# Kernel tuning notes

Measured on AMD Instinct MI355X. Metric: run time of the kernel, lower is better.

## Reference

```python
import jax, jax.numpy as jnp
import numpy as np

B, N, C_IN = 8, 2048, 2


def _pdist(x):
    # (B,N,N) pairwise euclidean distances
    d2 = jnp.sum((x[:, :, None, :] - x[:, None, :, :]) ** 2, axis=-1)
    return jnp.sqrt(d2)


def _knn_idx(x, k):
    d = _pdist(x)
    return jnp.argsort(d, axis=-1)[:, :, :k]  # includes self (dist 0)


def _ball_idx(x, radius, nsample):
    # deterministic ball query: neighbors with dist<=radius in ascending index
    # order, cyclically repeated if fewer than nsample (self is always in ball)
    d = _pdist(x)
    n = x.shape[1]
    mask = d <= radius
    ar = jnp.arange(n)
    order = jnp.argsort(jnp.where(mask, ar, ar + n), axis=-1)  # valid idx first
    count = jnp.sum(mask, axis=-1, keepdims=True)               # >= 1
    pos = jnp.arange(nsample)[None, None, :] % count            # (B,N,nsample)
    return jnp.take_along_axis(order, pos, axis=-1)


def _gather(x, idx):
    # x: (B,N,C), idx: (B,N,S) -> (B,N,S,C)
    return jax.vmap(lambda pts, ind: pts[ind])(x, idx)


def _mlp2(f, w0, b0, w1, b1):
    # 1x1 Conv2D stack == per-neighbor dense + relu
    f = jnp.maximum(jnp.einsum('bnsc,cd->bnsd', f, w0) + b0, 0.0)
    f = jnp.maximum(jnp.einsum('bnsc,cd->bnsd', f, w1) + b1, 0.0)
    return f


def _dense_relu(x, w, b):
    return jnp.maximum(x @ w + b, 0.0)


def _forward(x,
             sa1_w0, sa1_b0, sa1_w1, sa1_b1,
             sa2_w0, sa2_b0, sa2_w1, sa2_b1,
             sa3_w0, sa3_b0, sa3_w1, sa3_b1,
             fp1_w0, fp1_b0, fp1_w1, fp1_b1,
             fp2_w0, fp2_b0, fp2_w1, fp2_b1,
             fc1_w, fc1_b, fc2_w, fc2_b, out_w, out_b):
    # SA1: knn(k=32) on raw points, mlps [64,64], mean over neighbors
    x1 = jnp.mean(_mlp2(_gather(x, _knn_idx(x, 32)), sa1_w0, sa1_b0, sa1_w1, sa1_b1), axis=2)
    # SA2: ball query radius=0.2, nsample=32, mlps [128,128]
    x2 = jnp.mean(_mlp2(_gather(x1, _ball_idx(x1, 0.2, 32)), sa2_w0, sa2_b0, sa2_w1, sa2_b1), axis=2)
    # SA3: ball query radius=0.4, nsample=64, mlps [256,256]
    x3 = jnp.mean(_mlp2(_gather(x2, _ball_idx(x2, 0.4, 64)), sa3_w0, sa3_b0, sa3_w1, sa3_b1), axis=2)
    # FP1: dense mlps on local (x2), concat global (x3)
    h = _dense_relu(_dense_relu(x2, fp1_w0, fp1_b0), fp1_w1, fp1_b1)
    h = jnp.concatenate([h, x3], axis=-1)
    # FP2: dense mlps on local (x1), concat previous
    g = _dense_relu(_dense_relu(x1, fp2_w0, fp2_b0), fp2_w1, fp2_b1)
    g = jnp.concatenate([g, h], axis=-1)
    g = _dense_relu(g, fc1_w, fc1_b)
    g = _dense_relu(g, fc2_w, fc2_b)
    return jax.nn.sigmoid(g @ out_w + out_b)  # (B,N,1)


def setup_inputs() -> dict:
    key = jax.random.key(0)
    ks = iter(jax.random.split(key, 40))
    def w(i, o):
        return (jax.random.normal(next(ks), (i, o), jnp.float32) / np.sqrt(i)).astype(jnp.float32)
    def b(o):
        return jnp.zeros((o,), jnp.float32)
    inp = {
        'x': jax.random.normal(next(ks), (B, N, C_IN), jnp.float32),
        'sa1_w0': w(2, 64),   'sa1_b0': b(64),  'sa1_w1': w(64, 64),   'sa1_b1': b(64),
        'sa2_w0': w(64, 128), 'sa2_b0': b(128), 'sa2_w1': w(128, 128), 'sa2_b1': b(128),
        'sa3_w0': w(128, 256),'sa3_b0': b(256), 'sa3_w1': w(256, 256), 'sa3_b1': b(256),
        'fp1_w0': w(128, 512),'fp1_b0': b(512), 'fp1_w1': w(512, 512), 'fp1_b1': b(512),
        'fp2_w0': w(64, 256), 'fp2_b0': b(256), 'fp2_w1': w(256, 256), 'fp2_b1': b(256),
        'fc1_w': w(1024, 256),'fc1_b': b(256),
        'fc2_w': w(256, 128), 'fc2_b': b(128),
        'out_w': w(128, 1),   'out_b': b(1),
    }
    return inp


def reference(x,
              sa1_w0, sa1_b0, sa1_w1, sa1_b1,
              sa2_w0, sa2_b0, sa2_w1, sa2_b1,
              sa3_w0, sa3_b0, sa3_w1, sa3_b1,
              fp1_w0, fp1_b0, fp1_w1, fp1_b1,
              fp2_w0, fp2_b0, fp2_w1, fp2_b1,
              fc1_w, fc1_b, fc2_w, fc2_b, out_w, out_b):
    return _forward(x,
                    sa1_w0, sa1_b0, sa1_w1, sa1_b1,
                    sa2_w0, sa2_b0, sa2_w1, sa2_b1,
                    sa3_w0, sa3_b0, sa3_w1, sa3_b1,
                    fp1_w0, fp1_b0, fp1_w1, fp1_b1,
                    fp2_w0, fp2_b0, fp2_w1, fp2_b1,
                    fc1_w, fc1_b, fc2_w, fc2_b, out_w, out_b)
```

## Files before the change

kernel.cpp:

```cpp
#include <hip/hip_runtime.h>
#include <hip/hip_bf16.h>
#include <cstdint>

#define M_ROWS 16384

typedef __attribute__((ext_vector_type(8))) short short8;
typedef __attribute__((ext_vector_type(4))) float f32x4;

__device__ __forceinline__ unsigned long long umin64(unsigned long long a,
                                                     unsigned long long b) {
  return a < b ? a : b;
}

__global__ __launch_bounds__(256) void gemm_bias_relu(
    const float* __restrict__ X, int ldx,
    const float* __restrict__ W,
    const float* __restrict__ bias,
    float* __restrict__ Y, int ldy,
    int N, int K)
{
  __shared__ __align__(16) float As[16][68];
  __shared__ __align__(16) float Bs[16][68];
  int tid = threadIdx.x;
  int tx = tid & 15, ty = tid >> 4;
  int m0 = blockIdx.y << 6, n0 = blockIdx.x << 6;
  float acc[4][4] = {};
  for (int k0 = 0; k0 < K; k0 += 16) {
#pragma unroll
    for (int i = 0; i < 4; i++) {
      int idx = tid + (i << 8);
      int m = idx >> 4, k = idx & 15;
      As[k][m] = (k0 + k < K) ? X[(size_t)(m0 + m) * ldx + k0 + k] : 0.f;
    }
#pragma unroll
    for (int i = 0; i < 4; i++) {
      int idx = tid + (i << 8);
      int n = idx & 63, k = idx >> 6;
      Bs[k][n] = (k0 + k < K) ? W[(size_t)(k0 + k) * N + n0 + n] : 0.f;
    }
    __syncthreads();
#pragma unroll
    for (int k = 0; k < 16; k++) {
      float4 a4 = *(const float4*)&As[k][ty << 2];
      float4 b4 = *(const float4*)&Bs[k][tx << 2];
      float av[4] = {a4.x, a4.y, a4.z, a4.w};
      float bv[4] = {b4.x, b4.y, b4.z, b4.w};
#pragma unroll
      for (int i = 0; i < 4; i++)
#pragma unroll
        for (int j = 0; j < 4; j++)
          acc[i][j] += av[i] * bv[j];
    }
    __syncthreads();
  }
  float4 bb = *(const float4*)&bias[n0 + (tx << 2)];
  float bv[4] = {bb.x, bb.y, bb.z, bb.w};
#pragma unroll
  for (int i = 0; i < 4; i++) {
    int m = m0 + (ty << 2) + i;
    float4 o;
    o.x = fmaxf(acc[i][0] + bv[0], 0.f);
    o.y = fmaxf(acc[i][1] + bv[1], 0.f);
    o.z = fmaxf(acc[i][2] + bv[2], 0.f);
    o.w = fmaxf(acc[i][3] + bv[3], 0.f);
    *(float4*)&Y[(size_t)m * ldy + n0 + (tx << 2)] = o;
  }
}

__global__ __launch_bounds__(256) void sa1_fused(
    const float* __restrict__ x,
    const float* __restrict__ w0,
    const float* __restrict__ b0,
    const float* __restrict__ w1,
    const float* __restrict__ b1,
    float* __restrict__ G1)
{
  __shared__ __align__(16) float Ts[64][68];
  __shared__ __align__(16) float Ws[64][68];
  __shared__ float xs[64][2];
  __shared__ float w0s[2][64];
  __shared__ float b0s[64];
  int tid = threadIdx.x;
  int m0 = blockIdx.x << 6;
  if (tid < 128) {
    ((float*)xs)[tid] = x[(size_t)m0 * 2 + tid];
  } else if (tid < 192) {
    int n = tid - 128;
    w0s[0][n] = w0[n];
    b0s[n] = b0[n];
  } else {
    int n = tid - 192;
    w0s[1][n] = w0[64 + n];
  }
#pragma unroll
  for (int i = 0; i < 16; i++) {
    int idx = tid + (i << 8);
    int k = idx >> 6, n = idx & 63;
    Ws[k][n] = w1[(size_t)k * 64 + n];
  }
  __syncthreads();
#pragma unroll
  for (int i = 0; i < 16; i++) {
    int idx = tid + (i << 8);
    int m = idx >> 6, n = idx & 63;
    float acc = 0.f;
    acc += xs[m][0] * w0s[0][n];
    acc += xs[m][1] * w0s[1][n];
    Ts[n][m] = fmaxf(acc + b0s[n], 0.f);
  }
  __syncthreads();
  int tx = tid & 15, ty = tid >> 4;
  float acc[4][4] = {};
  for (int k = 0; k < 64; k++) {
    float4 a4 = *(const float4*)&Ts[k][ty << 2];
    float4 b4 = *(const float4*)&Ws[k][tx << 2];
    float av[4] = {a4.x, a4.y, a4.z, a4.w};
    float bv[4] = {b4.x, b4.y, b4.z, b4.w};
#pragma unroll
    for (int i = 0; i < 4; i++)
#pragma unroll
      for (int j = 0; j < 4; j++)
        acc[i][j] += av[i] * bv[j];
  }
  float4 bb = *(const float4*)&b1[tx << 2];
  float bv[4] = {bb.x, bb.y, bb.z, bb.w};
#pragma unroll
  for (int i = 0; i < 4; i++) {
    int m = m0 + (ty << 2) + i;
    float4 o;
    o.x = fmaxf(acc[i][0] + bv[0], 0.f);
    o.y = fmaxf(acc[i][1] + bv[1], 0.f);
    o.z = fmaxf(acc[i][2] + bv[2], 0.f);
    o.w = fmaxf(acc[i][3] + bv[3], 0.f);
    *(float4*)&G1[(size_t)m * 64 + (tx << 2)] = o;
  }
}

struct TJobs {
  const float* W[8];
  __hip_bfloat16* Wt[8];
  int K[8], N[8], bx[8], off[8];
};

__global__ __launch_bounds__(256) void transpose_cast_all(TJobs jb)
{
  __shared__ float tile[32][33];
  int bid = blockIdx.x;
  int j = 0;
#pragma unroll
  for (int t = 1; t < 8; t++)
    if (bid >= jb.off[t]) j = t;
  int rel = bid - jb.off[j];
  int K = jb.K[j], N = jb.N[j];
  const float* W = jb.W[j];
  __hip_bfloat16* Wt = jb.Wt[j];
  int n0 = (rel % jb.bx[j]) << 5, k0 = (rel / jb.bx[j]) << 5;
  int c = threadIdx.x & 31, i0 = threadIdx.x >> 5;
#pragma unroll
  for (int p = 0; p < 4; p++) {
    int i = i0 + p * 8;
    tile[i][c] = W[(size_t)(k0 + i) * N + n0 + c];
  }
  __syncthreads();
#pragma unroll
  for (int p = 0; p < 4; p++) {
    int r = i0 + p * 8;
    Wt[(size_t)(n0 + r) * K + k0 + c] = (__hip_bfloat16)tile[c][r];
  }
}

template <bool OUT_BF16>
__global__ __launch_bounds__(256) void gemm_mfma(
    const __hip_bfloat16* __restrict__ A, int lda,
    const __hip_bfloat16* __restrict__ Wt, int ldw,
    const float* __restrict__ bias,
    void* __restrict__ Y, int ldy, int N, int K)
{
  __shared__ __align__(16) short As[128][40];
  __shared__ __align__(16) short Bs[128][40];
  int tid = threadIdx.x;
  int wave = tid >> 6, lane = tid & 63;
  int quad = lane >> 4, l16 = lane & 15;
  int m0 = blockIdx.y << 7, n0 = blockIdx.x << 7;
  int wm = (wave >> 1) << 6, wn = (wave & 1) << 6;
  f32x4 acc[4][4] = {};
  const short* Ag = (const short*)A;
  const short* Bg = (const short*)Wt;
  int srow = tid >> 2, sq = tid & 3;
  for (int k0 = 0; k0 < K; k0 += 32) {
#pragma unroll
    for (int h = 0; h < 2; h++) {
      int r = srow + (h << 6);
      uint4 va = *(const uint4*)&Ag[(size_t)(m0 + r) * lda + k0 + sq * 8];
      *(uint4*)&As[r][sq * 8] = va;
      uint4 vb = *(const uint4*)&Bg[(size_t)(n0 + r) * ldw + k0 + sq * 8];
      *(uint4*)&Bs[r][sq * 8] = vb;
    }
    __syncthreads();
    short8 a[4], b[4];
#pragma unroll
    for (int mi = 0; mi < 4; mi++)
      a[mi] = *(const short8*)&As[wm + mi * 16 + l16][quad * 8];
#pragma unroll
    for (int ni = 0; ni < 4; ni++)
      b[ni] = *(const short8*)&Bs[wn + ni * 16 + l16][quad * 8];
#pragma unroll
    for (int mi = 0; mi < 4; mi++)
#pragma unroll
      for (int ni = 0; ni < 4; ni++)
        acc[mi][ni] = __builtin_amdgcn_mfma_f32_16x16x32_bf16(
            a[mi], b[ni], acc[mi][ni], 0, 0, 0);
    __syncthreads();
  }
  float bn[4];
#pragma unroll
  for (int ni = 0; ni < 4; ni++) bn[ni] = bias[n0 + wn + ni * 16 + l16];
#pragma unroll
  for (int mi = 0; mi < 4; mi++)
#pragma unroll
    for (int ni = 0; ni < 4; ni++) {
      int n = n0 + wn + ni * 16 + l16;
#pragma unroll
      for (int r = 0; r < 4; r++) {
        int m = m0 + wm + mi * 16 + quad * 4 + r;
        float v = fmaxf(acc[mi][ni][r] + bn[ni], 0.f);
        if (OUT_BF16)
          ((__hip_bfloat16*)Y)[(size_t)m * ldy + n] = (__hip_bfloat16)v;
        else
          ((float*)Y)[(size_t)m * ldy + n] = v;
      }
    }
}

struct GJobs {
  const short* A[3];
  const short* W[3];
  const float* bias[3];
  __hip_bfloat16* Y[3];
  int lda[3], ldw[3], ldy[3], N[3], K[3], xt[3], off[3];
};

__global__ __launch_bounds__(256) void gemm_mfma_multi(GJobs g)
{
  __shared__ __align__(16) short As[128][40];
  __shared__ __align__(16) short Bs[128][40];
  int bid = blockIdx.x;
  int j = 0;
#pragma unroll
  for (int t = 1; t < 3; t++)
    if (bid >= g.off[t]) j = t;
  int rel = bid - g.off[j];
  int xt = g.xt[j];
  int m0 = (rel / xt) << 7, n0 = (rel % xt) << 7;
  int lda = g.lda[j], ldw = g.ldw[j], ldy = g.ldy[j], K = g.K[j];
  const short* Ag = g.A[j];
  const short* Bg = g.W[j];
  const float* bias = g.bias[j];
  __hip_bfloat16* Y = g.Y[j];

  int tid = threadIdx.x;
  int wave = tid >> 6, lane = tid & 63;
  int quad = lane >> 4, l16 = lane & 15;
  int wm = (wave >> 1) << 6, wn = (wave & 1) << 6;
  f32x4 acc[4][4] = {};
  int srow = tid >> 2, sq = tid & 3;
  for (int k0 = 0; k0 < K; k0 += 32) {
#pragma unroll
    for (int h = 0; h < 2; h++) {
      int r = srow + (h << 6);
      uint4 va = *(const uint4*)&Ag[(size_t)(m0 + r) * lda + k0 + sq * 8];
      *(uint4*)&As[r][sq * 8] = va;
      uint4 vb = *(const uint4*)&Bg[(size_t)(n0 + r) * ldw + k0 + sq * 8];
      *(uint4*)&Bs[r][sq * 8] = vb;
    }
    __syncthreads();
    short8 a[4], b[4];
#pragma unroll
    for (int mi = 0; mi < 4; mi++)
      a[mi] = *(const short8*)&As[wm + mi * 16 + l16][quad * 8];
#pragma unroll
    for (int ni = 0; ni < 4; ni++)
      b[ni] = *(const short8*)&Bs[wn + ni * 16 + l16][quad * 8];
#pragma unroll
    for (int mi = 0; mi < 4; mi++)
#pragma unroll
      for (int ni = 0; ni < 4; ni++)
        acc[mi][ni] = __builtin_amdgcn_mfma_f32_16x16x32_bf16(
            a[mi], b[ni], acc[mi][ni], 0, 0, 0);
    __syncthreads();
  }
  float bn[4];
#pragma unroll
  for (int ni = 0; ni < 4; ni++) bn[ni] = bias[n0 + wn + ni * 16 + l16];
#pragma unroll
  for (int mi = 0; mi < 4; mi++)
#pragma unroll
    for (int ni = 0; ni < 4; ni++) {
      int n = n0 + wn + ni * 16 + l16;
#pragma unroll
      for (int r = 0; r < 4; r++) {
        int m = m0 + wm + mi * 16 + quad * 4 + r;
        float v = fmaxf(acc[mi][ni][r] + bn[ni], 0.f);
        Y[(size_t)m * ldy + n] = (__hip_bfloat16)v;
      }
    }
}

__global__ __launch_bounds__(256) void gemm_fc2_out(
    const __hip_bfloat16* __restrict__ A,
    const __hip_bfloat16* __restrict__ Wt,
    const float* __restrict__ bias,
    const float* __restrict__ wout,
    const float* __restrict__ bout,
    float* __restrict__ out)
{
  __shared__ __align__(16) short As[128][40];
  __shared__ __align__(16) short Bs[128][40];
  __shared__ float red[128][2];
  const int N = 128, K = 256, lda = 256, ldw = 256;
  int tid = threadIdx.x;
  int wave = tid >> 6, lane = tid & 63;
  int quad = lane >> 4, l16 = lane & 15;
  int m0 = blockIdx.y << 7;
  int wm = (wave >> 1) << 6, wn = (wave & 1) << 6;
  f32x4 acc[4][4] = {};
  const short* Ag = (const short*)A;
  const short* Bg = (const short*)Wt;
  int srow = tid >> 2, sq = tid & 3;
  for (int k0 = 0; k0 < K; k0 += 32) {
#pragma unroll
    for (int h = 0; h < 2; h++) {
      int r = srow + (h << 6);
      uint4 va = *(const uint4*)&Ag[(size_t)(m0 + r) * lda + k0 + sq * 8];
      *(uint4*)&As[r][sq * 8] = va;
      uint4 vb = *(const uint4*)&Bg[(size_t)(r % N) * ldw + k0 + sq * 8];
      *(uint4*)&Bs[r][sq * 8] = vb;
    }
    __syncthreads();
    short8 a[4], b[4];
#pragma unroll
    for (int mi = 0; mi < 4; mi++)
      a[mi] = *(const short8*)&As[wm + mi * 16 + l16][quad * 8];
#pragma unroll
    for (int ni = 0; ni < 4; ni++)
      b[ni] = *(const short8*)&Bs[wn + ni * 16 + l16][quad * 8];
#pragma unroll
    for (int mi = 0; mi < 4; mi++)
#pragma unroll
      for (int ni = 0; ni < 4; ni++)
        acc[mi][ni] = __builtin_amdgcn_mfma_f32_16x16x32_bf16(
            a[mi], b[ni], acc[mi][ni], 0, 0, 0);
    __syncthreads();
  }
  float bn[4], wo[4];
#pragma unroll
  for (int ni = 0; ni < 4; ni++) {
    int n = wn + ni * 16 + l16;
    bn[ni] = bias[n];
    wo[ni] = wout[n];
  }
  float sacc[4][4];
#pragma unroll
  for (int mi = 0; mi < 4; mi++)
#pragma unroll
    for (int r = 0; r < 4; r++) {
      float s = 0.f;
#pragma unroll
      for (int ni = 0; ni < 4; ni++)
        s += fmaxf(acc[mi][ni][r] + bn[ni], 0.f) * wo[ni];
      sacc[mi][r] = s;
    }
#pragma unroll
  for (int off = 1; off < 16; off <<= 1)
#pragma unroll
    for (int mi = 0; mi < 4; mi++)
#pragma unroll
      for (int r = 0; r < 4; r++)
        sacc[mi][r] += __shfl_xor(sacc[mi][r], off);
  int wp = wave & 1;
  if (l16 == 0) {
#pragma unroll
    for (int mi = 0; mi < 4; mi++)
#pragma unroll
      for (int r = 0; r < 4; r++)
        red[wm + mi * 16 + quad * 4 + r][wp] = sacc[mi][r];
  }
  __syncthreads();
  if (tid < 128) {
    float s = red[tid][0] + red[tid][1] + bout[0];
    out[(size_t)(m0 + tid)] = 1.f / (1.f + expf(-s));
  }
}

__global__ __launch_bounds__(256) void knn_mean4(
    const float* __restrict__ X,
    const float* __restrict__ G1,
    float* __restrict__ X1,
    __hip_bfloat16* __restrict__ X1b,
    __hip_bfloat16* __restrict__ X1lo,
    float* __restrict__ nrmX1)
{
  int qb = blockIdx.x << 2;
  int base = qb & ~2047;
  int tid = threadIdx.x;
  int wave = tid >> 6, lane = tid & 63;
  __shared__ unsigned long long lmins[4][256];
  __shared__ unsigned long long qmins[4][64];
  __shared__ unsigned long long thr[4];
  __shared__ unsigned long long surv[4][1024];
  __shared__ int scnt[4];
  __shared__ int selidx[4][32];
  if (tid < 4) scnt[tid] = 0;
  float xj[8], yj[8];
#pragma unroll
  for (int u = 0; u < 8; u++) {
    int j = (u << 8) + tid;
    float2 c = *(const float2*)&X[(size_t)(base + j) * 2];
    xj[u] = c.x;
    yj[u] = c.y;
  }
  unsigned long long key[4][8];
#pragma unroll
  for (int g = 0; g < 4; g++) {
    float qx = X[(size_t)(qb + g) * 2];
    float qy = X[(size_t)(qb + g) * 2 + 1];
    unsigned long long lm = ~0ull;
#pragma unroll
    for (int u = 0; u < 8; u++) {
      float dx = xj[u] - qx;
      float dy = yj[u] - qy;
      float d2 = dx * dx + dy * dy;
      key[g][u] = ((unsigned long long)__float_as_uint(d2) << 32) |
                  (unsigned)((u << 8) + tid);
      lm = umin64(lm, key[g][u]);
    }
    lmins[g][tid] = lm;
  }
  __syncthreads();
  {
    int g = wave;
    unsigned long long qm =
        umin64(umin64(lmins[g][lane], lmins[g][lane + 64]),
               umin64(lmins[g][lane + 128], lmins[g][lane + 192]));
    qmins[g][lane] = qm;
    int rank = 0;
    for (int i = 0; i < 64; i++) rank += (qmins[g][i] < qm);
    if (rank == 31) thr[g] = qm;
  }
  __syncthreads();
#pragma unroll
  for (int g = 0; g < 4; g++) {
    unsigned long long T = thr[g];
#pragma unroll
    for (int u = 0; u < 8; u++) {
      if (key[g][u] <= T) {
        int p = atomicAdd(&scnt[g], 1);
        surv[g][p] = key[g][u];
      }
    }
  }
  __syncthreads();
  {
    int g = wave;
    int s = scnt[g];
    for (int i = lane; i < s; i += 64) {
      unsigned long long c = surv[g][i];
      int r = 0;
      for (int j2 = 0; j2 < s; j2++) r += (surv[g][j2] < c);
      if (r < 32) selidx[g][r] = (int)(c & 0xffffffffULL);
    }
  }
  __syncthreads();
  {
    int g = wave;
    float acc = 0.f;
#pragma unroll 8
    for (int sI = 0; sI < 32; sI++)
      acc += G1[(size_t)(base + selidx[g][sI]) * 64 + lane];
    float v = acc * (1.0f / 32.0f);
    int q = qb + g;
    X1[(size_t)q * 64 + lane] = v;
    __hip_bfloat16 hi = (__hip_bfloat16)v;
    X1b[(size_t)q * 64 + lane] = hi;
    X1lo[(size_t)q * 64 + lane] = (__hip_bfloat16)(v - (float)hi);
    float nv = v * v;
#pragma unroll
    for (int off = 32; off > 0; off >>= 1) nv += __shfl_down(nv, off);
    if (lane == 0) nrmX1[q] = nv;
  }
}

template <int C>
__global__ __launch_bounds__(256) void ball_mask_mfma(
    const float* __restrict__ F32,
    const __hip_bfloat16* __restrict__ Fhi,
    const __hip_bfloat16* __restrict__ Flo,
    const float* __restrict__ nrm,
    unsigned long long* __restrict__ mask,
    float r2)
{
  __shared__ __align__(16) short Qh[128][40];
  __shared__ __align__(16) short Ql[128][40];
  __shared__ __align__(16) short Ch[128][40];
  __shared__ __align__(16) short Cl[128][40];
  __shared__ unsigned int tw[128][4];
  __shared__ float nqs[128], ncs[128];
  int tid = threadIdx.x;
  int p = blockIdx.x;
  int qt = 0;
  while (p >= 16 - qt) { p -= 16 - qt; qt++; }
  int ct = qt + p;
  int b0 = blockIdx.y << 11;
  int q0 = b0 + (qt << 7), c0 = b0 + (ct << 7);
  tw[tid >> 1][(tid & 1) * 2] = 0;
  tw[tid >> 1][(tid & 1) * 2 + 1] = 0;
  if (tid < 128) nqs[tid] = nrm[q0 + tid];
  else ncs[tid - 128] = nrm[c0 + tid - 128];

  int wave = tid >> 6, lane = tid & 63;
  int quad = lane >> 4, l16 = lane & 15;
  int wm = (wave >> 1) << 6, wn = (wave & 1) << 6;
  f32x4 acc[4][4] = {};
  const short* QH = (const short*)Fhi;
  const short* QL = (const short*)Flo;
  int srow = tid >> 2, sq = tid & 3;
  for (int k0 = 0; k0 < C; k0 += 32) {
#pragma unroll
    for (int h = 0; h < 2; h++) {
      int r = srow + (h << 6);
      *(uint4*)&Qh[r][sq * 8] = *(const uint4*)&QH[(size_t)(q0 + r) * C + k0 + sq * 8];
      *(uint4*)&Ql[r][sq * 8] = *(const uint4*)&QL[(size_t)(q0 + r) * C + k0 + sq * 8];
      *(uint4*)&Ch[r][sq * 8] = *(const uint4*)&QH[(size_t)(c0 + r) * C + k0 + sq * 8];
      *(uint4*)&Cl[r][sq * 8] = *(const uint4*)&QL[(size_t)(c0 + r) * C + k0 + sq * 8];
    }
    __syncthreads();
    short8 ah[4], al[4];
#pragma unroll
    for (int mi = 0; mi < 4; mi++) {
      ah[mi] = *(const short8*)&Qh[wm + mi * 16 + l16][quad * 8];
      al[mi] = *(const short8*)&Ql[wm + mi * 16 + l16][quad * 8];
    }
#pragma unroll
    for (int ni = 0; ni < 4; ni++) {
      short8 bh = *(const short8*)&Ch[wn + ni * 16 + l16][quad * 8];
      short8 bl = *(const short8*)&Cl[wn + ni * 16 + l16][quad * 8];
#pragma unroll
      for (int mi = 0; mi < 4; mi++) {
        acc[mi][ni] = __builtin_amdgcn_mfma_f32_16x16x32_bf16(ah[mi], bh, acc[mi][ni], 0, 0, 0);
        acc[mi][ni] = __builtin_amdgcn_mfma_f32_16x16x32_bf16(ah[mi], bl, acc[mi][ni], 0, 0, 0);
        acc[mi][ni] = __builtin_amdgcn_mfma_f32_16x16x32_bf16(al[mi], bh, acc[mi][ni], 0, 0, 0);
      }
    }
    __syncthreads();
  }
  unsigned long long memb = 0, fb = 0;
#pragma unroll
  for (int mi = 0; mi < 4; mi++)
#pragma unroll
    for (int ni = 0; ni < 4; ni++)
#pragma unroll
      for (int r = 0; r < 4; r++) {
        int e = (mi << 4) | (ni << 2) | r;
        float nqv = nqs[wm + mi * 16 + quad * 4 + r];
        float ncv = ncs[wn + ni * 16 + l16];
        float d2a = nqv + ncv - 2.f * acc[mi][ni][r];
        float eps = 4.0e-5f * (nqv + ncv) + 1.0e-6f;
        if (d2a < r2 - eps) memb |= 1ull << e;
        else if (d2a <= r2 + eps) fb |= 1ull << e;
      }
  while (fb) {
    int e = __builtin_ctzll(fb);
    fb &= fb - 1;
    int mi = e >> 4, ni = (e >> 2) & 3, r = e & 3;
    int qrow = q0 + wm + mi * 16 + quad * 4 + r;
    int ccol = c0 + wn + ni * 16 + l16;
    float a2 = 0.f;
    for (int k = 0; k < C; k++) {
      float d = F32[(size_t)qrow * C + k] - F32[(size_t)ccol * C + k];
      a2 = fmaf(d, d, a2);
    }
    if (a2 <= r2) memb |= 1ull << e;
  }
#pragma unroll
  for (int ni = 0; ni < 4; ni++) {
    int cl = wn + ni * 16 + l16;
    unsigned int w0b = 0, w1b = 0;
#pragma unroll
    for (int mi = 0; mi < 4; mi++)
#pragma unroll
      for (int r = 0; r < 4; r++)
        if (memb & (1ull << ((mi << 4) | (ni << 2) | r))) {
          unsigned int bitpos = ((mi & 1) << 4) | (quad << 2) | r;
          if (mi < 2) w0b |= 1u << bitpos;
          else w1b |= 1u << bitpos;
        }
    if (w0b) atomicOr(&tw[cl][(wm >> 5)], w0b);
    if (w1b) atomicOr(&tw[cl][(wm >> 5) + 1], w1b);
  }
  __syncthreads();
  {
    int row = tid >> 1, half = tid & 1;
    int wq = row >> 5, sb = row & 31;
    unsigned int lo = 0, hi = 0;
    for (int j = 0; j < 32; j++) {
      lo |= ((tw[half * 64 + j][wq] >> sb) & 1u) << j;
      hi |= ((tw[half * 64 + 32 + j][wq] >> sb) & 1u) << j;
    }
    mask[(size_t)(q0 + row) * 32 + (ct << 1) + half] =
        ((unsigned long long)hi << 32) | lo;
  }
  if (qt != ct) {
    int row = tid >> 1, word = tid & 1;
    unsigned long long v = (unsigned long long)tw[row][word * 2] |
                           ((unsigned long long)tw[row][word * 2 + 1] << 32);
    mask[(size_t)(c0 + row) * 32 + (qt << 1) + word] = v;
  }
}

template <typename TIn>
__global__ void ball_gather_kernel(
    const unsigned long long* __restrict__ mask,
    const TIn* __restrict__ H, int CH,
    float* __restrict__ Yf, __hip_bfloat16* __restrict__ Yb,
    __hip_bfloat16* __restrict__ Ylo, float* __restrict__ nrm,
    int ldy, int S)
{
  int q = blockIdx.x;
  int base = q & ~2047;
  int tid = threadIdx.x;
  __shared__ int idxl[64];
  __shared__ float wtab[64];
  __shared__ float npart[4];
  __shared__ int scount;
  if (tid < 32) {
    unsigned long long w = mask[(size_t)q * 32 + tid];
    int cnt = __popcll(w);
    int inc = cnt;
#pragma unroll
    for (int off = 1; off < 32; off <<= 1) {
      int o = __shfl_up(inc, off);
      if (tid >= off) inc += o;
    }
    if (tid == 31) scount = inc;
    int p = inc - cnt;
    while (w && p < 64) {
      int j = (tid << 6) + __builtin_ctzll(w);
      w &= w - 1;
      idxl[p++] = j;
    }
  }
  __syncthreads();
  int c = scount;
  if (tid < 64) {
    int p = tid;
    int cnt = (p < c && p < S) ? ((S - 1 - p) / c + 1) : 0;
    wtab[p] = (float)cnt / (float)S;
  }
  __syncthreads();
  float acc = 0.f;
  int lim = c < S ? c : S;
#pragma unroll 8
  for (int s = 0; s < lim; s++)
    acc += wtab[s] * (float)H[(size_t)(base + idxl[s]) * CH + tid];
  if (Yf) Yf[(size_t)q * ldy + tid] = acc;
  if (Yb) Yb[(size_t)q * ldy + tid] = (__hip_bfloat16)acc;
  if (Ylo) {
    __hip_bfloat16 hi = (__hip_bfloat16)acc;
    Ylo[(size_t)q * ldy + tid] = (__hip_bfloat16)(acc - (float)hi);
  }
  if (nrm) {
    float nv = acc * acc;
#pragma unroll
    for (int off = 32; off > 0; off >>= 1) nv += __shfl_down(nv, off);
    if ((tid & 63) == 0) npart[tid >> 6] = nv;
    __syncthreads();
    if (tid == 0) {
      float t = 0.f;
      for (int w = 0; w < (blockDim.x >> 6); w++) t += npart[w];
      nrm[q] = t;
    }
  }
}

extern "C" void kernel_launch(void* const* d_in, const int* in_sizes, int n_in,
                              void* d_out, int out_size, void* d_ws,
                              size_t ws_size, hipStream_t stream)
{
  const float* x      = (const float*)d_in[0];
  const float* sa1_w0 = (const float*)d_in[1];
  const float* sa1_b0 = (const float*)d_in[2];
  const float* sa1_w1 = (const float*)d_in[3];
  const float* sa1_b1 = (const float*)d_in[4];
  const float* sa2_w0 = (const float*)d_in[5];
  const float* sa2_b0 = (const float*)d_in[6];
  const float* sa2_w1 = (const float*)d_in[7];
  const float* sa2_b1 = (const float*)d_in[8];
  const float* sa3_w0 = (const float*)d_in[9];
  const float* sa3_b0 = (const float*)d_in[10];
  const float* sa3_w1 = (const float*)d_in[11];
  const float* sa3_b1 = (const float*)d_in[12];
  const float* fp1_w0 = (const float*)d_in[13];
  const float* fp1_b0 = (const float*)d_in[14];
  const float* fp1_w1 = (const float*)d_in[15];
  const float* fp1_b1 = (const float*)d_in[16];
  const float* fp2_w0 = (const float*)d_in[17];
  const float* fp2_b0 = (const float*)d_in[18];
  const float* fp2_w1 = (const float*)d_in[19];
  const float* fp2_b1 = (const float*)d_in[20];
  const float* fc1_w  = (const float*)d_in[21];
  const float* fc1_b  = (const float*)d_in[22];
  const float* fc2_w  = (const float*)d_in[23];
  const float* fc2_b  = (const float*)d_in[24];
  const float* out_w  = (const float*)d_in[25];
  const float* out_b  = (const float*)d_in[26];
  float* out = (float*)d_out;

  const size_t M = M_ROWS;
  float* ws = (float*)d_ws;
  float* T   = ws;
  float* G1  = ws + M * 256;
  float* X1  = ws + M * 320;
  float* X2  = ws + M * 384;
  float* H2  = ws + M * 512;
  __hip_bfloat16* H3b16 = (__hip_bfloat16*)(ws + M * 640);
  unsigned long long* MASK = (unsigned long long*)(ws + M * 896);
  __hip_bfloat16* X1b = (__hip_bfloat16*)(ws + M * 960);
  __hip_bfloat16* X2b = (__hip_bfloat16*)(ws + M * 992);
  __hip_bfloat16* TB0 = (__hip_bfloat16*)(ws + M * 1056);
  __hip_bfloat16* TB1 = (__hip_bfloat16*)(ws + M * 1184);
  __hip_bfloat16* TB2 = (__hip_bfloat16*)(ws + M * 1440);
  __hip_bfloat16* G   = (__hip_bfloat16*)(ws + M * 1568);
  __hip_bfloat16* H3b = (__hip_bfloat16*)(ws + M * 2080);
  __hip_bfloat16* WB  = (__hip_bfloat16*)(ws + M * 2208);
  __hip_bfloat16* X1lo = (__hip_bfloat16*)(ws + M * 2240);
  __hip_bfloat16* X2lo = (__hip_bfloat16*)(ws + M * 2272);
  float* nrmX1 = ws + M * 2336;
  float* nrmX2 = ws + M * 2337;
  if (ws_size < (size_t)M * 2340 * sizeof(float)) return;
  __hip_bfloat16* w_sa3_0 = WB;
  __hip_bfloat16* w_sa3_1 = w_sa3_0 + 32768;
  __hip_bfloat16* w_fp1_0 = w_sa3_1 + 65536;
  __hip_bfloat16* w_fp1_1 = w_fp1_0 + 65536;
  __hip_bfloat16* w_fp2_0 = w_fp1_1 + 262144;
  __hip_bfloat16* w_fp2_1 = w_fp2_0 + 16384;
  __hip_bfloat16* w_fc1   = w_fp2_1 + 65536;
  __hip_bfloat16* w_fc2   = w_fc1 + 262144;

  dim3 blk(256);
  TJobs jb;
  const float* srcs[8] = {sa3_w0, sa3_w1, fp1_w0, fp1_w1, fp2_w0, fp2_w1, fc1_w, fc2_w};
  __hip_bfloat16* dsts[8] = {w_sa3_0, w_sa3_1, w_fp1_0, w_fp1_1, w_fp2_0, w_fp2_1, w_fc1, w_fc2};
  int Ks[8] = {128, 256, 128, 512, 64, 256, 1024, 256};
  int Ns[8] = {256, 256, 512, 512, 256, 256, 256, 128};
  int off = 0;
  for (int i = 0; i < 8; i++) {
    jb.W[i] = srcs[i]; jb.Wt[i] = dsts[i];
    jb.K[i] = Ks[i]; jb.N[i] = Ns[i];
    jb.bx[i] = Ns[i] >> 5;
    jb.off[i] = off;
    off += (Ns[i] >> 5) * (Ks[i] >> 5);
  }
  transpose_cast_all<<<off, blk, 0, stream>>>(jb);

  sa1_fused<<<256, blk, 0, stream>>>(x, sa1_w0, sa1_b0, sa1_w1, sa1_b1, G1);
  knn_mean4<<<4096, 256, 0, stream>>>(x, G1, X1, X1b, X1lo, nrmX1);
  gemm_bias_relu<<<dim3(2, 256), blk, 0, stream>>>(X1, 64, sa2_w0, sa2_b0, T, 128, 128, 64);
  gemm_bias_relu<<<dim3(2, 256), blk, 0, stream>>>(T, 128, sa2_w1, sa2_b1, H2, 128, 128, 128);
  ball_mask_mfma<64><<<dim3(136, 8), blk, 0, stream>>>(X1, X1b, X1lo, nrmX1, MASK, 0.2f * 0.2f);
  ball_gather_kernel<float><<<16384, 128, 0, stream>>>(MASK, H2, 128, X2, X2b, X2lo, nrmX2, 128, 32);
  ball_mask_mfma<128><<<dim3(136, 8), blk, 0, stream>>>(X2, X2b, X2lo, nrmX2, MASK, 0.4f * 0.4f);
  {
    GJobs g1;
    g1.A[0] = (const short*)X2b; g1.W[0] = (const short*)w_sa3_0; g1.bias[0] = sa3_b0;
    g1.Y[0] = TB0; g1.lda[0] = 128; g1.ldw[0] = 128; g1.ldy[0] = 256; g1.N[0] = 256; g1.K[0] = 128;
    g1.A[1] = (const short*)X2b; g1.W[1] = (const short*)w_fp1_0; g1.bias[1] = fp1_b0;
    g1.Y[1] = TB1; g1.lda[1] = 128; g1.ldw[1] = 128; g1.ldy[1] = 512; g1.N[1] = 512; g1.K[1] = 128;
    g1.A[2] = (const short*)X1b; g1.W[2] = (const short*)w_fp2_0; g1.bias[2] = fp2_b0;
    g1.Y[2] = TB2; g1.lda[2] = 64; g1.ldw[2] = 64; g1.ldy[2] = 256; g1.N[2] = 256; g1.K[2] = 64;
    int tot1 = 0;
    for (int i = 0; i < 3; i++) {
      g1.xt[i] = g1.N[i] >> 7;
      g1.off[i] = tot1;
      tot1 += g1.xt[i] * 128;
    }
    gemm_mfma_multi<<<tot1, blk, 0, stream>>>(g1);

    GJobs g2;
    g2.A[0] = (const short*)TB0; g2.W[0] = (const short*)w_sa3_1; g2.bias[0] = sa3_b1;
    g2.Y[0] = H3b16; g2.lda[0] = 256; g2.ldw[0] = 256; g2.ldy[0] = 256; g2.N[0] = 256; g2.K[0] = 256;
    g2.A[1] = (const short*)TB1; g2.W[1] = (const short*)w_fp1_1; g2.bias[1] = fp1_b1;
    g2.Y[1] = G + 256; g2.lda[1] = 512; g2.ldw[1] = 512; g2.ldy[1] = 1024; g2.N[1] = 512; g2.K[1] = 512;
    g2.A[2] = (const short*)TB2; g2.W[2] = (const short*)w_fp2_1; g2.bias[2] = fp2_b1;
    g2.Y[2] = G; g2.lda[2] = 256; g2.ldw[2] = 256; g2.ldy[2] = 1024; g2.N[2] = 256; g2.K[2] = 256;
    int tot2 = 0;
    for (int i = 0; i < 3; i++) {
      g2.xt[i] = g2.N[i] >> 7;
      g2.off[i] = tot2;
      tot2 += g2.xt[i] * 128;
    }
    gemm_mfma_multi<<<tot2, blk, 0, stream>>>(g2);
  }
  ball_gather_kernel<__hip_bfloat16><<<16384, 256, 0, stream>>>(
      MASK, H3b16, 256, nullptr, G + 768, nullptr, nullptr, 1024, 64);
  gemm_mfma<true><<<dim3(2, 128), blk, 0, stream>>>(G, 1024, w_fc1, 1024, fc1_b, H3b, 256, 256, 1024);
  gemm_fc2_out<<<dim3(1, 128), blk, 0, stream>>>(H3b, w_fc2, fc2_b, out_w, out_b, out);
}
```

Before: 383.1 us.

## Shrink kNN survivor buffer with overflow fallback and remap blocks across batches

The kNN selection kernel's survivor buffer drops from 1024 to 256 entries per query, which cuts LDS use and may allow more resident blocks. A rare overflow path reuses the lmins array as a 1024-entry scratch buffer and reranks that query block-wide. Both kNN and ball-gather kernels also remap block indices so that consecutive blocks land on different batches, spreading per-batch data across XCDs and caches. The fallback adds block-wide syncs under divergent control and extra code, and the remap changes L2 locality.

```diff
diff --git a/kernel.cpp b/kernel.cpp
--- a/kernel.cpp
+++ b/kernel.cpp
@@ -400,14 +400,15 @@
     __hip_bfloat16* __restrict__ X1lo,
     float* __restrict__ nrmX1)
 {
-  int qb = blockIdx.x << 2;
+  int blk = blockIdx.x;
+  int qb = ((blk & 7) << 11) + ((blk >> 3) << 2);
   int base = qb & ~2047;
   int tid = threadIdx.x;
   int wave = tid >> 6, lane = tid & 63;
   __shared__ unsigned long long lmins[4][256];
   __shared__ unsigned long long qmins[4][64];
   __shared__ unsigned long long thr[4];
-  __shared__ unsigned long long surv[4][1024];
+  __shared__ unsigned long long surv[4][256];
   __shared__ int scnt[4];
   __shared__ int selidx[4][32];
   if (tid < 4) scnt[tid] = 0;
@@ -455,22 +456,50 @@
     for (int u = 0; u < 8; u++) {
       if (key[g][u] <= T) {
         int p = atomicAdd(&scnt[g], 1);
-        surv[g][p] = key[g][u];
+        if (p < 256) surv[g][p] = key[g][u];
       }
     }
   }
   __syncthreads();
+  int ovf[4] = {scnt[0], scnt[1], scnt[2], scnt[3]};
   {
     int g = wave;
-    int s = scnt[g];
-    for (int i = lane; i < s; i += 64) {
-      unsigned long long c = surv[g][i];
-      int r = 0;
-      for (int j2 = 0; j2 < s; j2++) r += (surv[g][j2] < c);
-      if (r < 32) selidx[g][r] = (int)(c & 0xffffffffULL);
-    }
-  }
-  __syncthreads();
+    int s = ovf[g];
+    if (s <= 256) {
+      for (int i = lane; i < s; i += 64) {
+        unsigned long long c = surv[g][i];
+        int r = 0;
+        for (int j2 = 0; j2 < s; j2++) r += (surv[g][j2] < c);
+        if (r < 32) selidx[g][r] = (int)(c & 0xffffffffULL);
+      }
+    }
+  }
+  if (ovf[0] > 256 || ovf[1] > 256 || ovf[2] > 256 || ovf[3] > 256) {
+    unsigned long long* ob = &lmins[0][0];
+    for (int g = 0; g < 4; g++) {
+      if (ovf[g] <= 256) continue;
+      __syncthreads();
+      if (tid == 0) scnt[g] = 0;
+      __syncthreads();
+      unsigned long long T = thr[g];
+#pragma unroll
+      for (int u = 0; u < 8; u++) {
+        if (key[g][u] <= T) {
+          int p = atomicAdd(&scnt[g], 1);
+          ob[p] = key[g][u];
+        }
+      }
+      __syncthreads();
+      int s2 = scnt[g];
+      for (int i = tid; i < s2; i += 256) {
+        unsigned long long c = ob[i];
+        int r = 0;
+        for (int j2 = 0; j2 < s2; j2++) r += (ob[j2] < c);
+        if (r < 32) selidx[g][r] = (int)(c & 0xffffffffULL);
+      }
+    }
+    __syncthreads();
+  }
   {
     int g = wave;
     float acc = 0.f;
@@ -625,7 +654,8 @@
     __hip_bfloat16* __restrict__ Ylo, float* __restrict__ nrm,
     int ldy, int S)
 {
-  int q = blockIdx.x;
+  int blk = blockIdx.x;
+  int q = ((blk & 7) << 11) + (blk >> 3);
   int base = q & ~2047;
   int tid = threadIdx.x;
   __shared__ int idxl[64];
```

After: 369.4 us. -3.6%, faster.
